# Kernel tuning notes

Hardware: AMD Instinct MI355X
Metric: run time of the kernel (lower is better)

## Reference

```python
import jax, jax.numpy as jnp
import numpy as np
import math

NUM_HEADS = 16
ROPE_BASE = 10000.0


def _rope_tables(T, head_dim, dtype=jnp.float32):
    pos = jnp.arange(T, dtype=jnp.float32)
    inv_freq = 1.0 / (ROPE_BASE ** (jnp.arange(0, head_dim, 2, dtype=jnp.float32) / head_dim))
    ang = pos[:, None] * inv_freq[None, :]  # (T, D/2)
    return jnp.cos(ang).astype(dtype), jnp.sin(ang).astype(dtype)


def _apply_rope(x, cos, sin):
    # x: (B, T, H, D); rotate interleaved pairs, position indexed along T
    B, T, H, D = x.shape
    xr = x.reshape(B, T, H, D // 2, 2)
    xe, xo = xr[..., 0], xr[..., 1]
    c = cos[None, :, None, :]  # (1, T, 1, D/2)
    s = sin[None, :, None, :]
    re = xe * c - xo * s
    im = xe * s + xo * c
    return jnp.stack([re, im], axis=-1).reshape(B, T, H, D)


def setup_inputs() -> dict:
    key = jax.random.key(0)
    k1, k2, k3 = jax.random.split(key, 3)
    B, T, C = 2, 2048, 1024
    x = jax.random.normal(k1, (B, T, C), dtype=jnp.float32)
    w_qkv = jax.random.normal(k2, (C, 3 * C), dtype=jnp.float32) * (1.0 / math.sqrt(C))
    w_out = jax.random.normal(k3, (C, C), dtype=jnp.float32) * (1.0 / math.sqrt(C))
    return {"x": x, "w_qkv": w_qkv, "w_out": w_out}


def reference(x, w_qkv, w_out):
    B, T, C = x.shape
    H = NUM_HEADS
    D = C // H
    qkv = jnp.einsum('btc,cf->btf', x, w_qkv)  # (B, T, 3C)
    q, k, v = jnp.split(qkv, 3, axis=-1)
    q = q.reshape(B, T, H, D)
    k = k.reshape(B, T, H, D)
    v = v.reshape(B, T, H, D)
    cos, sin = _rope_tables(T, D)
    q = _apply_rope(q, cos, sin)
    k = _apply_rope(k, cos, sin)
    # (B, H, T, T) scores with causal mask
    att = jnp.einsum('bqhd,bkhd->bhqk', q, k) * (1.0 / math.sqrt(D))
    causal = jnp.tril(jnp.ones((T, T), dtype=bool))
    att = jnp.where(causal[None, None], att, -jnp.inf)
    att = jax.nn.softmax(att, axis=-1)
    out = jnp.einsum('bhqk,bkhd->bqhd', att, v).reshape(B, T, C)
    return jnp.einsum('btc,cd->btd', out, w_out)
```

## Files before the change

### kernel.cpp

```cpp
#include <hip/hip_runtime.h>
#include <stdint.h>


#define B_ 2
#define T_ 2048
#define C_ 1024
#define H_ 16
#define D_ 64
#define F_ 3072
#define M_ 4096

typedef unsigned short u16;
typedef unsigned int u32;
typedef u16 u16x2 __attribute__((ext_vector_type(2)));
typedef u16 u16x4 __attribute__((ext_vector_type(4)));
typedef u16 u16x8 __attribute__((ext_vector_type(8)));
typedef __bf16 bf16x8 __attribute__((ext_vector_type(8)));
typedef float f32x4 __attribute__((ext_vector_type(4)));

#define AS1 __attribute__((address_space(1)))
#define AS3 __attribute__((address_space(3)))

__device__ __forceinline__ float b2f(u16 u) {
  union { unsigned int i; float f; } v; v.i = ((unsigned int)u) << 16; return v.f;
}
__device__ __forceinline__ u16 f2b(float f) {
  unsigned int u = __float_as_uint(f);
  u += 0x7fffu + ((u >> 16) & 1u);
  return (u16)(u >> 16);
}
__device__ __forceinline__ bf16x8 u2b8(u16x8 v) {
  union { u16x8 u; bf16x8 b; } x; x.u = v; return x.b;
}

__global__ __launch_bounds__(256) void prep_kernel(const float* __restrict__ x,
                                                   const float* __restrict__ w_qkv,
                                                   const float* __restrict__ w_out,
                                                   u16* __restrict__ xb,
                                                   u16* __restrict__ wqkvT,
                                                   u16* __restrict__ woutT,
                                                   float2* __restrict__ csT) {
  __shared__ float tile[32][33];
  const int bid = blockIdx.x;
  const int tid = threadIdx.x;

  if (bid < 4096) {
    int i = bid * 256 + tid;
    float4 v = ((const float4*)x)[i];
    u16x4 r;
    r[0] = f2b(v.x); r[1] = f2b(v.y); r[2] = f2b(v.z); r[3] = f2b(v.w);
    ((u16x4*)xb)[i] = r;
  } else if (bid < 8192) {
    const float* in;  u16* out;  int R, Ccol, b;
    if (bid < 7168) { in = w_qkv; out = wqkvT; R = C_; Ccol = F_; b = bid - 4096; }
    else            { in = w_out; out = woutT; R = C_; Ccol = C_; b = bid - 7168; }
    int nbx = Ccol / 32;
    int c0 = (b % nbx) * 32, r0 = (b / nbx) * 32;
    int tx = tid & 31, ty = tid >> 5;
    #pragma unroll
    for (int i = 0; i < 32; i += 8)
      tile[ty + i][tx] = in[(size_t)(r0 + ty + i) * Ccol + c0 + tx];
    __syncthreads();
    #pragma unroll
    for (int i = 0; i < 32; i += 8)
      out[(size_t)(c0 + ty + i) * R + r0 + tx] = f2b(tile[tx][ty + i]);
  } else {
    int idx = (bid - 8192) * 256 + tid;
    int t = idx >> 5, i = idx & 31;
    float inv_freq = powf(10000.0f, -(float)(2 * i) / 64.0f);
    float ang = (float)t * inv_freq;
    csT[idx] = make_float2(cosf(ang), sinf(ang));
  }
}

template <int MODE>
__global__ __launch_bounds__(256) void gemm_bt_kernel(const u16* __restrict__ A,
                                                      const u16* __restrict__ Bt,
                                                      float* __restrict__ Cm,
                                                      u16* __restrict__ qr,
                                                      u16* __restrict__ kr,
                                                      u16* __restrict__ vrp,
                                                      const float2* __restrict__ csT,
                                                      int M, int N, int K) {
  __shared__ u16 sA[3][128 * 32];
  __shared__ u16 sB[3][128 * 32];
  const int tid = threadIdx.x;
  const int lane = tid & 63;
  const int wv = tid >> 6;
  const int wr = wv >> 1, wc = wv & 1;
  const int l16 = lane & 15, lq = lane >> 4;

  const int gx = gridDim.x;
  const int nwg = gx * gridDim.y;
  const int flat = blockIdx.y * gx + blockIdx.x;
  const int swz = (flat & 7) * (nwg >> 3) + (flat >> 3);
  const int rowBase = (swz / gx) * 128;
  const int colBase = (swz % gx) * 128;

  f32x4 acc[4][4] = {};

  const int e0 = wv * 1024 + lane * 8;

#define GSTAGE(buf, kk)                                                          \
  {                                                                              \
    _Pragma("unroll")                                                            \
    for (int s = 0; s < 2; ++s) {                                                \
      int e = e0 + s * 512;                                                      \
      int r = e >> 5, ccc = e & 31;                                              \
      __builtin_amdgcn_global_load_lds(                                          \
          (const AS1 u32*)(A + (size_t)(rowBase + r) * K + (kk) + ccc),          \
          (AS3 u32*)&sA[buf][wv * 1024 + s * 512], 16, 0, 0);                    \
      __builtin_amdgcn_global_load_lds(                                          \
          (const AS1 u32*)(Bt + (size_t)(colBase + r) * K + (kk) + ccc),         \
          (AS3 u32*)&sB[buf][wv * 1024 + s * 512], 16, 0, 0);                    \
    }                                                                            \
  }

  const int NT = K >> 5;
  GSTAGE(0, 0);
  if (NT > 1) GSTAGE(1, 32);

  int cur = 0;
  for (int kt = 0; kt < NT; ++kt) {
    if (kt + 1 < NT) {
      asm volatile("s_waitcnt vmcnt(4)" ::: "memory");
    } else {
      asm volatile("s_waitcnt vmcnt(0)" ::: "memory");
    }
    __builtin_amdgcn_s_barrier();

    if (kt + 2 < NT) {
      int nb = cur + 2; if (nb >= 3) nb -= 3;
      GSTAGE(nb, (kt + 2) * 32);
    }

    bf16x8 af[4], bf[4];
    #pragma unroll
    for (int m = 0; m < 4; ++m)
      af[m] = u2b8(*(const u16x8*)&sA[cur][(wr * 64 + m * 16 + l16) * 32 + lq * 8]);
    #pragma unroll
    for (int n = 0; n < 4; ++n)
      bf[n] = u2b8(*(const u16x8*)&sB[cur][(wc * 64 + n * 16 + l16) * 32 + lq * 8]);
    __builtin_amdgcn_s_setprio(1);
    #pragma unroll
    for (int m = 0; m < 4; ++m)
      #pragma unroll
      for (int n = 0; n < 4; ++n)
        acc[m][n] = __builtin_amdgcn_mfma_f32_16x16x32_bf16(af[m], bf[n], acc[m][n], 0, 0, 0);
    __builtin_amdgcn_s_setprio(0);

    cur = (cur + 1 == 3) ? 0 : cur + 1;
  }
#undef GSTAGE

  if constexpr (MODE == 0) {
    #pragma unroll
    for (int m = 0; m < 4; ++m)
      #pragma unroll
      for (int n = 0; n < 4; ++n) {
        int row = rowBase + wr * 64 + m * 16 + lq * 4;
        int col = colBase + wc * 64 + n * 16 + l16;
        #pragma unroll
        for (int j = 0; j < 4; ++j)
          Cm[(size_t)(row + j) * N + col] = acc[m][n][j];
      }
  } else {
    const int which = colBase >> 10;
    const int head = ((colBase + wc * 64) >> 6) & 15;
    const float QSC = 0.125f * 1.44269504f;
    u16* const dst = (which == 0) ? qr : (which == 1) ? kr : vrp;
    #pragma unroll
    for (int m = 0; m < 4; ++m) {
      #pragma unroll
      for (int n = 0; n < 4; ++n) {
        const int d0 = n * 16 + l16;
        #pragma unroll
        for (int j = 0; j < 4; ++j) {
          int row = rowBase + wr * 64 + m * 16 + lq * 4 + j;
          int b = row >> 11, t = row & 2047;
          float v = acc[m][n][j];
          u16 outv;
          if (which == 2) {
            outv = f2b(v);
          } else {
            float p = __shfl_xor(v, 1);
            float2 cs = csT[t * 32 + (d0 >> 1)];
            float r = (l16 & 1) ? fmaf(p, cs.y, v * cs.x)
                                : fmaf(-p, cs.y, v * cs.x);
            if (which == 0) r *= QSC;
            outv = f2b(r);
          }
          dst[((size_t)(b * 16 + head) * 2048 + t) * 64 + d0] = outv;
        }
      }
    }
  }
}

__global__ __launch_bounds__(256, 4) void attn_mfma_kernel(const u16* __restrict__ qr,
                                                           const u16* __restrict__ kr,
                                                           const u16* __restrict__ vr,
                                                           u16* __restrict__ ao) {
  constexpr int LDVT = 72;
  __shared__ u16 sK[2][64 * 64];
  __shared__ u16 sVt[2][64 * LDVT];

  const int tid = threadIdx.x;
  const int lane = tid & 63;
  const int w = tid >> 6;
  const int l16 = lane & 15, lq = lane >> 4;
  const int bh = blockIdx.x;
  const int qt = (int)gridDim.y - 1 - (int)blockIdx.y;
  const int qbase = qt * 64;
  const size_t hb = (size_t)bh * (T_ * D_);

  bf16x8 qv[2];
  #pragma unroll
  for (int dc = 0; dc < 2; ++dc) {
    int row = qbase + w * 16 + l16;
    qv[dc] = u2b8(*(const u16x8*)(qr + hb + (size_t)row * 64 + dc * 32 + lq * 8));
  }

  f32x4 o[4] = {};
  float mrow = -1e30f;
  float lrow = 0.0f;

  const int krow0 = w * 16 + (lane >> 3);
  const int ksrc = ((lane & 7) ^ (lane >> 3)) * 8;
  const int vkp = tid & 31;
  const int vdb = tid >> 5;
  const int vtr = ((vkp >> 4) & 1) * 32 + ((vkp >> 1) & 1) * 16 +
                  ((vkp >> 3) & 1) * 8 + ((vkp >> 2) & 1) * 4 + (vkp & 1) * 2;

  u16x8 rv0, rv1;
#define STAGEK(buf, k0s)                                                       \
  {                                                                            \
    _Pragma("unroll")                                                          \
    for (int s = 0; s < 2; ++s)                                                \
      __builtin_amdgcn_global_load_lds(                                        \
          (const AS1 u32*)(kr + hb + (size_t)((k0s) + krow0 + s * 8) * 64 + ksrc), \
          (AS3 u32*)&sK[buf][(w * 16 + s * 8) * 64], 16, 0, 0);                \
  }
#define LOADV(k0s)                                                             \
  {                                                                            \
    rv0 = *(const u16x8*)(vr + hb + (size_t)((k0s) + vtr) * 64 + vdb * 8);     \
    rv1 = *(const u16x8*)(vr + hb + (size_t)((k0s) + vtr + 1) * 64 + vdb * 8); \
  }
#define WRITEV(buf)                                                            \
  {                                                                            \
    _Pragma("unroll")                                                          \
    for (int u = 0; u < 8; ++u) {                                              \
      u16x2 pk; pk[0] = rv0[u]; pk[1] = rv1[u];                                \
      *(u16x2*)&sVt[buf][(vdb * 8 + u) * LDVT + 2 * vkp] = pk;                 \
    }                                                                          \
  }

  STAGEK(0, 0);
  LOADV(0);
  WRITEV(0);
  __syncthreads();

  const int nt = qt + 1;
  int cur = 0;
  for (int it = 0; it < nt; ++it) {
    const int k0 = it * 64;
    const bool more = (it + 1 < nt);
    if (more) {
      STAGEK(cur ^ 1, k0 + 64);
      LOADV(k0 + 64);
    }

    f32x4 accs[4] = {};
    __builtin_amdgcn_s_setprio(1);
    #pragma unroll
    for (int kt = 0; kt < 4; ++kt) {
      int chy = ((lq) ^ (l16 & 7)) * 8;
      int chz = ((4 + lq) ^ (l16 & 7)) * 8;
      bf16x8 kf0 = u2b8(*(const u16x8*)&sK[cur][(kt * 16 + l16) * 64 + chy]);
      bf16x8 kf1 = u2b8(*(const u16x8*)&sK[cur][(kt * 16 + l16) * 64 + chz]);
      accs[kt] = __builtin_amdgcn_mfma_f32_16x16x32_bf16(kf0, qv[0], accs[kt], 0, 0, 0);
      accs[kt] = __builtin_amdgcn_mfma_f32_16x16x32_bf16(kf1, qv[1], accs[kt], 0, 0, 0);
    }
    __builtin_amdgcn_s_setprio(0);

    const int qrow = qbase + w * 16 + l16;
    if (k0 + 63 > qbase + w * 16) {
      #pragma unroll
      for (int kt = 0; kt < 4; ++kt)
        #pragma unroll
        for (int j = 0; j < 4; ++j)
          if (k0 + kt * 16 + lq * 4 + j > qrow) accs[kt][j] = -1e30f;
    }
    float m0 = fmaxf(fmaxf(accs[0][0], accs[0][1]), fmaxf(accs[0][2], accs[0][3]));
    float m1 = fmaxf(fmaxf(accs[1][0], accs[1][1]), fmaxf(accs[1][2], accs[1][3]));
    float m2 = fmaxf(fmaxf(accs[2][0], accs[2][1]), fmaxf(accs[2][2], accs[2][3]));
    float m3 = fmaxf(fmaxf(accs[3][0], accs[3][1]), fmaxf(accs[3][2], accs[3][3]));
    float mx = fmaxf(fmaxf(m0, m1), fmaxf(m2, m3));
    mx = fmaxf(mx, __shfl_xor(mx, 16));
    mx = fmaxf(mx, __shfl_xor(mx, 32));

    if (!__all(mx <= mrow)) {
      float mnew = fmaxf(mrow, mx);
      float corr = __builtin_amdgcn_exp2f(mrow - mnew);
      lrow *= corr;
      mrow = mnew;
      f32x4 corrv;
      #pragma unroll
      for (int j = 0; j < 4; ++j) corrv[j] = __shfl(corr, lq * 4 + j);
      #pragma unroll
      for (int dt = 0; dt < 4; ++dt) o[dt] *= corrv;
    }
    const float mu = mrow;
    bf16x8 pb[2];
    float lsum = 0.0f;
    #pragma unroll
    for (int kt = 0; kt < 4; ++kt) {
      #pragma unroll
      for (int j = 0; j < 4; ++j) {
        float p = __builtin_amdgcn_exp2f(accs[kt][j] - mu);
        lsum += p;
        pb[kt >> 1][(kt & 1) * 4 + j] = (__bf16)p;
      }
    }
    lrow += lsum;

    __builtin_amdgcn_s_setprio(1);
    #pragma unroll
    for (int kc = 0; kc < 2; ++kc) {
      #pragma unroll
      for (int dt = 0; dt < 4; ++dt) {
        bf16x8 vt = u2b8(*(const u16x8*)&sVt[cur][(dt * 16 + l16) * LDVT + kc * 32 + lq * 8]);
        o[dt] = __builtin_amdgcn_mfma_f32_16x16x32_bf16(pb[kc], vt, o[dt], 0, 0, 0);
      }
    }
    __builtin_amdgcn_s_setprio(0);

    if (more) WRITEV(cur ^ 1);
    __syncthreads();
    cur ^= 1;
  }

  const int b = bh >> 4, h = bh & 15;
  float l = lrow;
  l += __shfl_xor(l, 16);
  l += __shfl_xor(l, 32);
  float linv = 1.0f / l;
  #pragma unroll
  for (int j = 0; j < 4; ++j) {
    float lj = __shfl(linv, lq * 4 + j);
    int row = qbase + w * 16 + lq * 4 + j;
    u16* orow = ao + ((size_t)(b * T_ + row)) * C_ + h * 64;
    #pragma unroll
    for (int dt = 0; dt < 4; ++dt)
      orow[dt * 16 + l16] = f2b(o[dt][j] * lj);
  }
}

extern "C" void kernel_launch(void* const* d_in, const int* in_sizes, int n_in,
                              void* d_out, int out_size, void* d_ws, size_t ws_size,
                              hipStream_t stream) {
  const float* x     = (const float*)d_in[0];
  const float* w_qkv = (const float*)d_in[1];
  const float* w_out = (const float*)d_in[2];
  float* out = (float*)d_out;
  char* ws = (char*)d_ws;

  u16* xb     = (u16*)(ws + 0);
  u16* wqkvT  = (u16*)(ws + 8388608);
  u16* woutT  = (u16*)(ws + 14680064);
  u16* qr     = (u16*)(ws + 41943040);
  u16* kr     = (u16*)(ws + 50331648);
  u16* vr     = (u16*)(ws + 58720256);
  u16* ao     = (u16*)(ws + 67108864);
  float2* csT = (float2*)(ws + 75497472);

  prep_kernel<<<8448, 256, 0, stream>>>(x, w_qkv, w_out, xb, wqkvT, woutT, csT);
  gemm_bt_kernel<2><<<dim3(F_ / 128, M_ / 128), 256, 0, stream>>>(
      xb, wqkvT, nullptr, qr, kr, vr, (const float2*)csT, M_, F_, C_);
  attn_mfma_kernel<<<dim3(B_ * H_, T_ / 64), 256, 0, stream>>>(qr, kr, vr, ao);
  gemm_bt_kernel<0><<<dim3(C_ / 128, M_ / 128), 256, 0, stream>>>(
      ao, woutT, out, nullptr, nullptr, nullptr, nullptr, M_, C_, C_);
}
```

Before: 126.2 us.

## Use dedicated 64x64-tile GEMM kernel for output projection

Replaces the 128x128-tile GEMM for the output projection (M=4096, N=1024) with a new 64x64-tile kernel. It uses a triple-buffered LDS pipeline with direct global-to-LDS loads and a swizzled block order. The smaller tile gives 1024 workgroups instead of 256, so the 256 CUs are better filled. The cost is lower data reuse per tile and more global traffic.

Measured after the change: 121.6 us, median of 2. 3.6% less time.

```diff
diff --git a/kernel.cpp b/kernel.cpp
--- a/kernel.cpp
+++ b/kernel.cpp
@@ -197,6 +197,89 @@
   }
 }
 
+__global__ __launch_bounds__(256) void gemm64_kernel(const u16* __restrict__ A,
+                                                     const u16* __restrict__ Bt,
+                                                     float* __restrict__ Cm,
+                                                     int M, int N, int K) {
+  __shared__ u16 sA[3][64 * 32];
+  __shared__ u16 sB[3][64 * 32];
+  const int tid = threadIdx.x;
+  const int lane = tid & 63;
+  const int wv = tid >> 6;
+  const int wr = wv >> 1, wc = wv & 1;
+  const int l16 = lane & 15, lq = lane >> 4;
+
+  const int gx = gridDim.x;
+  const int nwg = gx * gridDim.y;
+  const int flat = blockIdx.y * gx + blockIdx.x;
+  const int swz = (flat & 7) * (nwg >> 3) + (flat >> 3);
+  const int rowBase = (swz / gx) * 64;
+  const int colBase = (swz % gx) * 64;
+
+  f32x4 acc[2][2] = {};
+
+  const int e0 = wv * 512 + lane * 8;
+
+#define GSTAGE64(buf, kk)                                                        \
+  {                                                                              \
+    int r = e0 >> 5, ccc = e0 & 31;                                              \
+    __builtin_amdgcn_global_load_lds(                                            \
+        (const AS1 u32*)(A + (size_t)(rowBase + r) * K + (kk) + ccc),            \
+        (AS3 u32*)&sA[buf][wv * 512], 16, 0, 0);                                 \
+    __builtin_amdgcn_global_load_lds(                                            \
+        (const AS1 u32*)(Bt + (size_t)(colBase + r) * K + (kk) + ccc),           \
+        (AS3 u32*)&sB[buf][wv * 512], 16, 0, 0);                                 \
+  }
+
+  const int NT = K >> 5;
+  GSTAGE64(0, 0);
+  if (NT > 1) GSTAGE64(1, 32);
+
+  int cur = 0;
+  for (int kt = 0; kt < NT; ++kt) {
+    if (kt + 1 < NT) {
+      asm volatile("s_waitcnt vmcnt(2)" ::: "memory");
+    } else {
+      asm volatile("s_waitcnt vmcnt(0)" ::: "memory");
+    }
+    __builtin_amdgcn_s_barrier();
+
+    if (kt + 2 < NT) {
+      int nb = cur + 2; if (nb >= 3) nb -= 3;
+      GSTAGE64(nb, (kt + 2) * 32);
+    }
+
+    bf16x8 af[2], bf[2];
+    #pragma unroll
+    for (int m = 0; m < 2; ++m)
+      af[m] = u2b8(*(const u16x8*)&sA[cur][(wr * 32 + m * 16 + l16) * 32 + lq * 8]);
+    #pragma unroll
+    for (int n = 0; n < 2; ++n)
+      bf[n] = u2b8(*(const u16x8*)&sB[cur][(wc * 32 + n * 16 + l16) * 32 + lq * 8]);
+    __builtin_amdgcn_s_setprio(1);
+    #pragma unroll
+    for (int m = 0; m < 2; ++m)
+      #pragma unroll
+      for (int n = 0; n < 2; ++n)
+        acc[m][n] = __builtin_amdgcn_mfma_f32_16x16x32_bf16(af[m], bf[n], acc[m][n], 0, 0, 0);
+    __builtin_amdgcn_s_setprio(0);
+
+    cur = (cur + 1 == 3) ? 0 : cur + 1;
+  }
+#undef GSTAGE64
+
+  #pragma unroll
+  for (int m = 0; m < 2; ++m)
+    #pragma unroll
+    for (int n = 0; n < 2; ++n) {
+      int row = rowBase + wr * 32 + m * 16 + lq * 4;
+      int col = colBase + wc * 32 + n * 16 + l16;
+      #pragma unroll
+      for (int j = 0; j < 4; ++j)
+        Cm[(size_t)(row + j) * N + col] = acc[m][n][j];
+    }
+}
+
 __global__ __launch_bounds__(256, 4) void attn_mfma_kernel(const u16* __restrict__ qr,
                                                            const u16* __restrict__ kr,
                                                            const u16* __restrict__ vr,
@@ -378,6 +461,5 @@
   gemm_bt_kernel<2><<<dim3(F_ / 128, M_ / 128), 256, 0, stream>>>(
       xb, wqkvT, nullptr, qr, kr, vr, (const float2*)csT, M_, F_, C_);
   attn_mfma_kernel<<<dim3(B_ * H_, T_ / 64), 256, 0, stream>>>(qr, kr, vr, ao);
-  gemm_bt_kernel<0><<<dim3(C_ / 128, M_ / 128), 256, 0, stream>>>(
-      ao, woutT, out, nullptr, nullptr, nullptr, nullptr, M_, C_, C_);
-}
+  gemm64_kernel<<<dim3(C_ / 64, M_ / 64), 256, 0, stream>>>(ao, woutT, out, M_, C_, C_);
+}
```
